# Performance work log

Measured on AMD Instinct MI355X. Metric: run time of the kernel, lower is better.

## Reference

```python
import math
import jax, jax.numpy as jnp
import numpy as np

E = 1024
H = 16
DH = E // H
R = 8
ALPHA = 16
LORA_S = ALPHA / R

def build_slopes(h):
    start = 2 ** (-2 ** (-(math.log2(h) - 3)))
    return jnp.asarray([start * start ** i for i in range(h)], dtype=jnp.float32)

def setup_inputs() -> dict:
    key = jax.random.key(0)
    ks = jax.random.split(key, 12)
    B, T = 2, 2048
    x = jax.random.normal(ks[0], (B, T, E), dtype=jnp.float32)
    # nn.Linear weights: [out_f, in_f]; LoRA A: [out_f, r], B: [r, in_f]
    def lin(k):
        return jax.random.normal(k, (E, E), dtype=jnp.float32) / math.sqrt(E)
    inp = {
        "x": x,
        "Wq": lin(ks[1]), "Aq": jax.random.normal(ks[2], (E, R)) * 0.01, "Bq": jax.random.normal(ks[3], (R, E)) * 0.01,
        "Wk": lin(ks[4]), "Ak": jax.random.normal(ks[5], (E, R)) * 0.01, "Bk": jax.random.normal(ks[6], (R, E)) * 0.01,
        "Wv": lin(ks[7]), "Av": jax.random.normal(ks[8], (E, R)) * 0.01, "Bv": jax.random.normal(ks[9], (R, E)) * 0.01,
        "Wp": lin(ks[10]),
    }
    return inp

def _lora(x, W, A, Bm):
    # x @ W.T + (x @ B.T) @ A.T * s
    return x @ W.T + ((x @ Bm.T) @ A.T) * LORA_S

def reference(x, Wq, Aq, Bq, Wk, Ak, Bk, Wv, Av, Bv, Wp):
    B, T, _ = x.shape
    slopes = build_slopes(H)  # [H]
    q = _lora(x, Wq, Aq, Bq).reshape(B, T, H, DH).transpose(0, 2, 1, 3)  # [B,H,T,dh]
    k = _lora(x, Wk, Ak, Bk).reshape(B, T, H, DH).transpose(0, 2, 1, 3)
    v = _lora(x, Wv, Av, Bv).reshape(B, T, H, DH).transpose(0, 2, 1, 3)
    s = jnp.einsum("bhqd,bhkd->bhqk", q, k) / math.sqrt(DH)
    i = jnp.arange(T, dtype=jnp.float32)[:, None]
    j = jnp.arange(T, dtype=jnp.float32)[None, :]
    alibi = slopes[:, None, None] * (i - j)  # [H,T,T]
    mask = jnp.triu(jnp.full((T, T), -jnp.inf, dtype=jnp.float32), 1)
    s = s + alibi[None] + mask
    p = jax.nn.softmax(s, axis=-1)
    o = jnp.einsum("bhqk,bhkd->bhqd", p, v).transpose(0, 2, 1, 3).reshape(B, T, E)
    return o @ Wp.T
```

## Files before the change

### kernel.cpp

```cpp
#include <hip/hip_runtime.h>

typedef unsigned short u16;
typedef unsigned int   u32;
typedef __bf16 bf16_t;
typedef bf16_t bf16x8 __attribute__((ext_vector_type(8)));
typedef bf16_t bf16x2v __attribute__((ext_vector_type(2)));
typedef float  f32x4  __attribute__((ext_vector_type(4)));

#define E_DIM 1024
#define T_DIM 2048
#define H_NUM 16
#define DH 64
#define BT 4096
#define Y_LD 2048

__device__ __forceinline__ u16 f2bf(float f) {
  u32 u = __builtin_bit_cast(u32, f);
  u32 r = (u + 0x7fffu + ((u >> 16) & 1u)) >> 16;
  return (u16)r;
}
__device__ __forceinline__ float bf2f(u16 v) {
  u32 u = ((u32)v) << 16;
  return __builtin_bit_cast(float, u);
}

__device__ __forceinline__ float fexp2(float x) {
#if __has_builtin(__builtin_amdgcn_exp2f)
  return __builtin_amdgcn_exp2f(x);
#else
  return exp2f(x);
#endif
}

__device__ __forceinline__ int swz(int r, int c) {
  return r * 64 + (c ^ ((r & 7) << 3));
}

typedef __attribute__((address_space(3))) unsigned int as3_u32;
typedef const __attribute__((address_space(1))) unsigned int as1_u32;

__device__ __forceinline__ void async16(const u16* g, u16* l) {
  __builtin_amdgcn_global_load_lds((as1_u32*)g, (as3_u32*)l, 16, 0, 0);
}

__device__ __forceinline__ void waitvm0_barrier() {
  asm volatile("s_waitcnt vmcnt(0)" ::: "memory");
  __builtin_amdgcn_s_barrier();
  __builtin_amdgcn_sched_barrier(0);
}

__device__ __forceinline__ void waitall_barrier() {
  asm volatile("s_waitcnt vmcnt(0) lgkmcnt(0)" ::: "memory");
  __builtin_amdgcn_s_barrier();
  __builtin_amdgcn_sched_barrier(0);
}

__device__ __forceinline__ u32 pack2(float a, float b) {
  bf16x2v v;
  v[0] = (bf16_t)a;
  v[1] = (bf16_t)b;
  return __builtin_bit_cast(u32, v);
}

__device__ __forceinline__ void plswap(u32& a, u32& b) {
#if __has_builtin(__builtin_amdgcn_permlane32_swap)
  typedef u32 u32x2 __attribute__((ext_vector_type(2)));
  u32x2 r = __builtin_amdgcn_permlane32_swap(a, b, false, false);
  a = r[0];
  b = r[1];
#else
  asm volatile("v_permlane32_swap_b32 %0, %1" : "+v"(a), "+v"(b));
#endif
}

__device__ __forceinline__ void redist_pair(u32 A, u32 B, bool odd, u32& wj, u32& wj2) {
  plswap(A, B);
  u32 sA = __builtin_amdgcn_ds_swizzle(A, 0x401F);
  u32 sB = __builtin_amdgcn_ds_swizzle(B, 0x401F);
  wj  = odd ? sB : A;
  wj2 = odd ? B : sA;
}

__global__ __launch_bounds__(256) void k_prep(
    const float* __restrict__ x,
    const float* __restrict__ W0, const float* __restrict__ A0, const float* __restrict__ B0,
    const float* __restrict__ W1, const float* __restrict__ A1, const float* __restrict__ B1,
    const float* __restrict__ W2, const float* __restrict__ A2, const float* __restrict__ B2,
    const float* __restrict__ Wp,
    u16* __restrict__ xb, u16* __restrict__ Weff, u16* __restrict__ Wpb, float s0) {
  const int blk = blockIdx.x;
  const int tid = threadIdx.x;
  if (blk < 4096) {
    int i = (blk * 256 + tid) * 4;
    float4 v = *reinterpret_cast<const float4*>(x + i);
    u32 lo = (u32)f2bf(v.x) | ((u32)f2bf(v.y) << 16);
    u32 hi = (u32)f2bf(v.z) | ((u32)f2bf(v.w) << 16);
    *reinterpret_cast<uint2*>(xb + i) = make_uint2(lo, hi);
  } else if (blk < 7168) {
    int e4 = (blk - 4096) * 256 + tid;
    int m = e4 >> 18;
    int e = (e4 & 262143) * 4;
    const float* W  = (m == 0) ? W0 : (m == 1) ? W1 : W2;
    const float* A  = (m == 0) ? A0 : (m == 1) ? A1 : A2;
    const float* Bm = (m == 0) ? B0 : (m == 1) ? B1 : B2;
    const float sc  = (m == 0) ? s0 : 1.0f;
    int o = e >> 10, i = e & 1023;
    float4 wv = *reinterpret_cast<const float4*>(W + e);
    float acc[4] = {wv.x, wv.y, wv.z, wv.w};
#pragma unroll
    for (int r = 0; r < 8; ++r) {
      float a2 = 2.0f * A[o * 8 + r];
      float4 bv = *reinterpret_cast<const float4*>(Bm + r * 1024 + i);
      acc[0] += a2 * bv.x; acc[1] += a2 * bv.y; acc[2] += a2 * bv.z; acc[3] += a2 * bv.w;
    }
    u32 lo = (u32)f2bf(acc[0] * sc) | ((u32)f2bf(acc[1] * sc) << 16);
    u32 hi = (u32)f2bf(acc[2] * sc) | ((u32)f2bf(acc[3] * sc) << 16);
    *reinterpret_cast<uint2*>(Weff + (size_t)m * 1048576 + e) = make_uint2(lo, hi);
  } else {
    int i = ((blk - 7168) * 256 + tid) * 4;
    float4 v = *reinterpret_cast<const float4*>(Wp + i);
    u32 lo = (u32)f2bf(v.x) | ((u32)f2bf(v.y) << 16);
    u32 hi = (u32)f2bf(v.z) | ((u32)f2bf(v.w) << 16);
    *reinterpret_cast<uint2*>(Wpb + i) = make_uint2(lo, hi);
  }
}

__global__ __launch_bounds__(512) void k_gemm2(
    const u16* __restrict__ A, const u16* __restrict__ B,
    u16* __restrict__ C, u16* __restrict__ Vt, int K, int ldc) {
  __shared__ __align__(16) u16 As[2][8192];
  __shared__ __align__(16) u16 Bs[2][8192];
  const int tid  = threadIdx.x;
  const int lane = tid & 63;
  const int wave = tid >> 6;
  const int wr = wave >> 2;
  const int wc = wave & 3;
  const int m0 = blockIdx.y * 128;
  const int n0 = blockIdx.x * 128;
  const int lr = lane & 15;
  const int lk = (lane >> 4) * 8;
  const bool vmode = (n0 >= 2048);

  f32x4 acc[4][2] = {};

  auto stageg = [&](int bufi, int t) {
#pragma unroll
    for (int p = 0; p < 2; ++p) {
      const int off = (p * 8 + wave) * 512;
      const int e = off + lane * 8;
      const int r = e >> 6, c = e & 63;
      const int cs = c ^ ((r & 7) << 3);
      async16(&A[(size_t)(m0 + r) * K + t * 64 + cs], &As[bufi][off]);
      async16(&B[(size_t)(n0 + r) * K + t * 64 + cs], &Bs[bufi][off]);
    }
  };

  const int nt = K >> 6;
  stageg(0, 0);
  waitvm0_barrier();
  int buf = 0;

  for (int t = 0; t < nt; ++t) {
    if (t + 1 < nt) stageg(buf ^ 1, t + 1);
    __builtin_amdgcn_s_setprio(1);
#pragma unroll
    for (int kk = 0; kk < 2; ++kk) {
      bf16x8 af[4], bfr[2];
#pragma unroll
      for (int mi = 0; mi < 4; ++mi)
        af[mi] = *reinterpret_cast<const bf16x8*>(&As[buf][swz(wr * 64 + mi * 16 + lr, kk * 32 + lk)]);
#pragma unroll
      for (int ni = 0; ni < 2; ++ni)
        bfr[ni] = *reinterpret_cast<const bf16x8*>(&Bs[buf][swz(wc * 32 + ni * 16 + lr, kk * 32 + lk)]);
      if (vmode) {
#pragma unroll
        for (int mi = 0; mi < 4; ++mi)
#pragma unroll
          for (int ni = 0; ni < 2; ++ni)
            acc[mi][ni] = __builtin_amdgcn_mfma_f32_16x16x32_bf16(bfr[ni], af[mi], acc[mi][ni], 0, 0, 0);
      } else {
#pragma unroll
        for (int mi = 0; mi < 4; ++mi)
#pragma unroll
          for (int ni = 0; ni < 2; ++ni)
            acc[mi][ni] = __builtin_amdgcn_mfma_f32_16x16x32_bf16(af[mi], bfr[ni], acc[mi][ni], 0, 0, 0);
      }
    }
    __builtin_amdgcn_s_setprio(0);
    waitvm0_barrier();
    buf ^= 1;
  }

  const int rg = (lane >> 4) * 4;
  if (vmode) {
#pragma unroll
    for (int mi = 0; mi < 4; ++mi)
#pragma unroll
      for (int ni = 0; ni < 2; ++ni)
#pragma unroll
        for (int q = 0; q < 4; ++q) {
          int o = n0 - 2048 + wc * 32 + ni * 16 + rg + q;
          int h = o >> 6, d = o & 63;
          int rowm = m0 + wr * 64 + mi * 16 + lr;
          int b = rowm >> 11, t = rowm & 2047;
          Vt[(size_t)(((b << 4) + h) * 64 + d) * 2048 + t] = f2bf(acc[mi][ni][q]);
        }
  } else {
#pragma unroll
    for (int mi = 0; mi < 4; ++mi)
#pragma unroll
      for (int ni = 0; ni < 2; ++ni)
#pragma unroll
        for (int q = 0; q < 4; ++q) {
          int row = m0 + wr * 64 + mi * 16 + rg + q;
          int col = n0 + wc * 32 + ni * 16 + lr;
          C[(size_t)row * ldc + col] = f2bf(acc[mi][ni][q]);
        }
  }
}

__global__ __launch_bounds__(512) void k_projm(
    const u16* __restrict__ Og, const u16* __restrict__ Oa, const u16* __restrict__ Ob,
    const float* __restrict__ la, const float* __restrict__ lb,
    const u16* __restrict__ B, float* __restrict__ C) {
  __shared__ __align__(16) u16 As[2][8192];
  __shared__ __align__(16) u16 Bs[2][8192];
  const int tid  = threadIdx.x;
  const int lane = tid & 63;
  const int wave = tid >> 6;
  const int wr = wave >> 2, wc = wave & 3;
  const int m0 = blockIdx.y * 128;
  const int n0 = blockIdx.x * 128;
  const int lr = lane & 15;
  const int lk = (lane >> 4) * 8;
  const bool upper = (m0 & 2047) >= 1024;
  const int K = 1024;

  f32x4 acc[4][2] = {};

  auto stageg = [&](int bufi, int t) {
#pragma unroll
    for (int p = 0; p < 2; ++p) {
      const int off = (p * 8 + wave) * 512;
      const int e = off + lane * 8;
      const int r = e >> 6, c = e & 63;
      const int cs = c ^ ((r & 7) << 3);
      async16(&B[(size_t)(n0 + r) * K + t * 64 + cs], &Bs[bufi][off]);
      if (!upper) {
        async16(&Og[(size_t)(m0 + r) * K + t * 64 + cs], &As[bufi][off]);
      } else {
        const int rowg = m0 + r;
        const int bb = rowg >> 11, tl = (rowg & 2047) - 1024;
        const int li = (bb * 16 + t) * 1024 + tl;
        const float inv = 1.0f / (la[li] + lb[li]);
        size_t po = (size_t)(bb * 1024 + tl) * 1024 + t * 64 + cs;
        uint4 va = *reinterpret_cast<const uint4*>(Oa + po);
        uint4 vb = *reinterpret_cast<const uint4*>(Ob + po);
        const u16* pa = reinterpret_cast<const u16*>(&va);
        const u16* pb = reinterpret_cast<const u16*>(&vb);
        u16 o[8];
#pragma unroll
        for (int j = 0; j < 8; ++j) o[j] = f2bf((bf2f(pa[j]) + bf2f(pb[j])) * inv);
        *reinterpret_cast<uint4*>(&As[bufi][off + lane * 8]) =
            *reinterpret_cast<const uint4*>(o);
      }
    }
  };

  const int nt = K >> 6;
  stageg(0, 0);
  waitall_barrier();
  int buf = 0;

  for (int t = 0; t < nt; ++t) {
    if (t + 1 < nt) stageg(buf ^ 1, t + 1);
    __builtin_amdgcn_s_setprio(1);
#pragma unroll
    for (int kk = 0; kk < 2; ++kk) {
      bf16x8 af[4], bfr[2];
#pragma unroll
      for (int mi = 0; mi < 4; ++mi)
        af[mi] = *reinterpret_cast<const bf16x8*>(&As[buf][swz(wr * 64 + mi * 16 + lr, kk * 32 + lk)]);
#pragma unroll
      for (int ni = 0; ni < 2; ++ni)
        bfr[ni] = *reinterpret_cast<const bf16x8*>(&Bs[buf][swz(wc * 32 + ni * 16 + lr, kk * 32 + lk)]);
#pragma unroll
      for (int mi = 0; mi < 4; ++mi)
#pragma unroll
        for (int ni = 0; ni < 2; ++ni)
          acc[mi][ni] = __builtin_amdgcn_mfma_f32_16x16x32_bf16(af[mi], bfr[ni], acc[mi][ni], 0, 0, 0);
    }
    __builtin_amdgcn_s_setprio(0);
    waitall_barrier();
    buf ^= 1;
  }

  const int rg = (lane >> 4) * 4;
#pragma unroll
  for (int mi = 0; mi < 4; ++mi)
#pragma unroll
    for (int ni = 0; ni < 2; ++ni)
#pragma unroll
      for (int q = 0; q < 4; ++q) {
        int row = m0 + wr * 64 + mi * 16 + rg + q;
        int col = n0 + wc * 32 + ni * 16 + lr;
        C[(size_t)row * 1024 + col] = acc[mi][ni][q];
      }
}

__global__ __launch_bounds__(256) void k_attn8(
    const u16* __restrict__ Y, const u16* __restrict__ Vt, u16* __restrict__ Og,
    u16* __restrict__ Oa, u16* __restrict__ Ob,
    float* __restrict__ la, float* __restrict__ lb) {
  __shared__ __align__(16) u16 Ks[2][4096];
  __shared__ __align__(16) u16 Vs[2][4096];

  const int tid = threadIdx.x;
  const int lane = tid & 63;
  const int wave = tid >> 6;
  const int lr = lane & 15;
  const int lg = lane >> 4;
  const int lk = lg * 8;
  const bool odd = (lane & 16) != 0;

  const int orig = blockIdx.x;
  const int h   = 15 - (orig / 96);
  const int rem = orig % 96;
  const int c   = rem >> 1;
  const int b   = rem & 1;
  const int bh  = b * 16 + h;
  const int qt = (c < 16) ? (16 + c) : (47 - c);
  const int ks = (c >= 16 && c < 32) ? 16 : 0;
  int ke       = (c < 16) ? 15 : qt;

  const float LOG2E = 1.4426950408889634f;
  const float slope2 = exp2f(-0.5f * (float)(h + 1)) * LOG2E;

  const int Th = min(32, (int)(64.0f / slope2) / 64 + 1);
  ke = min(ke, Th - 1);

  if (ks > ke) {
    const int base = b * 1024 + (qt * 64 - 1024);
#pragma unroll
    for (int p = 0; p < 2; ++p) {
      int idx = p * 256 + tid;
      int rr = idx >> 3, cc8 = (idx & 7) * 8;
      uint4 z = {0, 0, 0, 0};
      *reinterpret_cast<uint4*>(&Ob[(size_t)(base + rr) * E_DIM + h * DH + cc8]) = z;
    }
    if (tid < 64) lb[bh * 1024 + (qt * 64 - 1024) + tid] = 0.f;
    return;
  }

  const u16* Kb = Y + (size_t)b * T_DIM * Y_LD + 1024 + h * DH;
  const u16* Vb = Vt + (size_t)bh * DH * T_DIM;

  bf16x8 qf[2];
  {
    const int qrow = qt * 64 + wave * 16 + lr;
#pragma unroll
    for (int kk = 0; kk < 2; ++kk)
      qf[kk] = *reinterpret_cast<const bf16x8*>(
          &Y[(size_t)(b * T_DIM + qrow) * Y_LD + h * DH + kk * 32 + lk]);
  }

  float nkb[16];
#pragma unroll
  for (int ni = 0; ni < 4; ++ni)
#pragma unroll
    for (int r = 0; r < 4; ++r)
      nkb[ni * 4 + r] = -slope2 * (float)(ni * 16 + lg * 4 + r) - 12.0f;

  bf16x8 ones;
#pragma unroll
  for (int jj = 0; jj < 8; ++jj) ones[jj] = (bf16_t)1.0f;

  f32x4 oacc[4] = {};
  f32x4 lacc = {};

  auto stage = [&](int bufi, int kt) {
    const int kv0 = kt * 64;
#pragma unroll
    for (int q = 0; q < 2; ++q) {
      const int off = (q * 4 + wave) * 512;
      const int e = off + lane * 8;
      const int r = e >> 6, cc = e & 63;
      const int cs = cc ^ ((r & 7) << 3);
      async16(Kb + (size_t)(kv0 + r) * Y_LD + cs, &Ks[bufi][off]);
      async16(Vb + (size_t)r * T_DIM + kv0 + cs, &Vs[bufi][off]);
    }
  };

  auto step = [&](int kt, int buf, bool DIAG) {
    f32x4 s[4] = {};
    __builtin_amdgcn_s_setprio(1);
#pragma unroll
    for (int kk = 0; kk < 2; ++kk)
#pragma unroll
      for (int ni = 0; ni < 4; ++ni) {
        bf16x8 kf = *reinterpret_cast<const bf16x8*>(&Ks[buf][swz(ni * 16 + lr, kk * 32 + lk)]);
        s[ni] = __builtin_amdgcn_mfma_f32_16x16x32_bf16(kf, qf[kk], s[ni], 0, 0, 0);
      }
    __builtin_amdgcn_s_setprio(0);
    const float ck = -slope2 * (float)(kt * 64);
    u32 pk[4][2];
#pragma unroll
    for (int ni = 0; ni < 4; ++ni) {
      float p[4];
#pragma unroll
      for (int r = 0; r < 4; ++r) {
        float sc = s[ni][r] + nkb[ni * 4 + r] + ck;
        if (DIAG && (ni * 16 + lg * 4 + r) > (wave * 16 + lr)) sc = -INFINITY;
        p[r] = fexp2(sc);
      }
      pk[ni][0] = pack2(p[0], p[1]);
      pk[ni][1] = pack2(p[2], p[3]);
    }
    uint4 PW[2];
#pragma unroll
    for (int kk = 0; kk < 2; ++kk) {
      redist_pair(pk[2 * kk][0], pk[2 * kk + 1][0], odd, PW[kk].x, PW[kk].z);
      redist_pair(pk[2 * kk][1], pk[2 * kk + 1][1], odd, PW[kk].y, PW[kk].w);
    }
    __builtin_amdgcn_s_setprio(1);
#pragma unroll
    for (int kk = 0; kk < 2; ++kk) {
      bf16x8 ph = __builtin_bit_cast(bf16x8, PW[kk]);
      lacc = __builtin_amdgcn_mfma_f32_16x16x32_bf16(ph, ones, lacc, 0, 0, 0);
#pragma unroll
      for (int f = 0; f < 4; ++f) {
        bf16x8 vf = *reinterpret_cast<const bf16x8*>(&Vs[buf][swz(f * 16 + lr, kk * 32 + lk)]);
        oacc[f] = __builtin_amdgcn_mfma_f32_16x16x32_bf16(ph, vf, oacc[f], 0, 0, 0);
      }
    }
    __builtin_amdgcn_s_setprio(0);
  };

  stage(0, ks);
  waitvm0_barrier();
  int buf = 0;
  for (int kt = ks; kt <= ke; ++kt) {
    if (kt < ke) stage(buf ^ 1, kt + 1);
    step(kt, buf, kt == qt);
    waitvm0_barrier();
    buf ^= 1;
  }

  if (c >= 32) {
    float linv[4];
#pragma unroll
    for (int r = 0; r < 4; ++r) linv[r] = 1.0f / lacc[r];
#pragma unroll
    for (int f = 0; f < 4; ++f)
#pragma unroll
      for (int r = 0; r < 4; ++r) {
        int q = qt * 64 + wave * 16 + lg * 4 + r;
        Og[(size_t)(b * T_DIM + q) * E_DIM + h * DH + f * 16 + lr] =
            f2bf(oacc[f][r] * linv[r]);
      }
  } else {
    u16* Op   = (c < 16) ? Oa : Ob;
    float* lp = (c < 16) ? la : lb;
#pragma unroll
    for (int f = 0; f < 4; ++f)
#pragma unroll
      for (int r = 0; r < 4; ++r) {
        int q = qt * 64 + wave * 16 + lg * 4 + r;
        Op[(size_t)(b * 1024 + (q - 1024)) * E_DIM + h * DH + f * 16 + lr] =
            f2bf(oacc[f][r]);
      }
    if (lr == 0) {
#pragma unroll
      for (int r = 0; r < 4; ++r) {
        int q = qt * 64 + wave * 16 + lg * 4 + r;
        lp[bh * 1024 + (q - 1024)] = lacc[r];
      }
    }
  }
}

extern "C" void kernel_launch(void* const* d_in, const int* in_sizes, int n_in,
                              void* d_out, int out_size, void* d_ws, size_t ws_size,
                              hipStream_t stream) {
  const float* x  = (const float*)d_in[0];
  const float* Wq = (const float*)d_in[1];
  const float* Aq = (const float*)d_in[2];
  const float* Bq = (const float*)d_in[3];
  const float* Wk = (const float*)d_in[4];
  const float* Ak = (const float*)d_in[5];
  const float* Bk = (const float*)d_in[6];
  const float* Wv = (const float*)d_in[7];
  const float* Av = (const float*)d_in[8];
  const float* Bv = (const float*)d_in[9];
  const float* Wp = (const float*)d_in[10];
  float* out = (float*)d_out;

  char* ws = (char*)d_ws;
  const size_t MB = 1048576;
  u16* xb   = (u16*)(ws);
  u16* Oa   = (u16*)(ws);
  u16* Ob   = (u16*)(ws + 4 * MB);
  u16* Weff = (u16*)(ws + 8 * MB);
  float* la = (float*)(ws + 8 * MB);
  float* lb = (float*)(ws + 8 * MB + 131072);
  u16* Yq   = (u16*)(ws + 14 * MB);
  u16* VtB  = (u16*)(ws + 30 * MB);
  u16* Wpb  = (u16*)(ws + 38 * MB);
  u16* Og   = (u16*)(ws + 40 * MB);

  const float ISQ2 = 0.125f * 1.4426950408889634f;

  k_prep<<<8192, 256, 0, stream>>>(x, Wq, Aq, Bq, Wk, Ak, Bk, Wv, Av, Bv, Wp,
                                   xb, Weff, Wpb, ISQ2);
  {
    dim3 grid(24, 32);
    k_gemm2<<<grid, 512, 0, stream>>>(xb, Weff, Yq, VtB, E_DIM, Y_LD);
  }
  k_attn8<<<1536, 256, 0, stream>>>(Yq, VtB, Og, Oa, Ob, la, lb);
  {
    dim3 grid(8, 32);
    k_projm<<<grid, 512, 0, stream>>>(Og, Oa, Ob, la, lb, Wpb, out);
  }
}
```

Before: 107.7 us.

## Triple-buffer attention K/V staging and halve output-projection tile width

The attention kernel moves from double to triple-buffered K/V tiles in shared memory, prefetching two tiles ahead and waiting with vmcnt(4) so that one tile's loads can stay in flight across the barrier. The output projection kernel switches from 128-wide to 64-wide N tiles, doubling the grid to 512 blocks for better CU occupancy on a grid that was small. In exchange, attention uses more LDS per block, which may reduce occupancy. The narrower projection tiles recompute the A-side Oa/Ob merge twice as often and load A twice as often.

```diff
diff --git a/kernel.cpp b/kernel.cpp
--- a/kernel.cpp
+++ b/kernel.cpp
@@ -45,6 +45,12 @@
 
 __device__ __forceinline__ void waitvm0_barrier() {
   asm volatile("s_waitcnt vmcnt(0)" ::: "memory");
+  __builtin_amdgcn_s_barrier();
+  __builtin_amdgcn_sched_barrier(0);
+}
+
+__device__ __forceinline__ void waitvm4_barrier() {
+  asm volatile("s_waitcnt vmcnt(4)" ::: "memory");
   __builtin_amdgcn_s_barrier();
   __builtin_amdgcn_sched_barrier(0);
 }
@@ -224,28 +230,34 @@
     const float* __restrict__ la, const float* __restrict__ lb,
     const u16* __restrict__ B, float* __restrict__ C) {
   __shared__ __align__(16) u16 As[2][8192];
-  __shared__ __align__(16) u16 Bs[2][8192];
+  __shared__ __align__(16) u16 Bs[2][4096];
   const int tid  = threadIdx.x;
   const int lane = tid & 63;
   const int wave = tid >> 6;
   const int wr = wave >> 2, wc = wave & 3;
   const int m0 = blockIdx.y * 128;
-  const int n0 = blockIdx.x * 128;
+  const int n0 = blockIdx.x * 64;
   const int lr = lane & 15;
   const int lk = (lane >> 4) * 8;
   const bool upper = (m0 & 2047) >= 1024;
   const int K = 1024;
 
-  f32x4 acc[4][2] = {};
+  f32x4 acc[4][1] = {};
 
   auto stageg = [&](int bufi, int t) {
+    {
+      const int off = wave * 512;
+      const int e = off + lane * 8;
+      const int r = e >> 6, c = e & 63;
+      const int cs = c ^ ((r & 7) << 3);
+      async16(&B[(size_t)(n0 + r) * K + t * 64 + cs], &Bs[bufi][off]);
+    }
 #pragma unroll
     for (int p = 0; p < 2; ++p) {
       const int off = (p * 8 + wave) * 512;
       const int e = off + lane * 8;
       const int r = e >> 6, c = e & 63;
       const int cs = c ^ ((r & 7) << 3);
-      async16(&B[(size_t)(n0 + r) * K + t * 64 + cs], &Bs[bufi][off]);
       if (!upper) {
         async16(&Og[(size_t)(m0 + r) * K + t * 64 + cs], &As[bufi][off]);
       } else {
@@ -277,18 +289,14 @@
     __builtin_amdgcn_s_setprio(1);
 #pragma unroll
     for (int kk = 0; kk < 2; ++kk) {
-      bf16x8 af[4], bfr[2];
+      bf16x8 af[4], bfr;
 #pragma unroll
       for (int mi = 0; mi < 4; ++mi)
         af[mi] = *reinterpret_cast<const bf16x8*>(&As[buf][swz(wr * 64 + mi * 16 + lr, kk * 32 + lk)]);
-#pragma unroll
-      for (int ni = 0; ni < 2; ++ni)
-        bfr[ni] = *reinterpret_cast<const bf16x8*>(&Bs[buf][swz(wc * 32 + ni * 16 + lr, kk * 32 + lk)]);
+      bfr = *reinterpret_cast<const bf16x8*>(&Bs[buf][swz(wc * 16 + lr, kk * 32 + lk)]);
 #pragma unroll
       for (int mi = 0; mi < 4; ++mi)
-#pragma unroll
-        for (int ni = 0; ni < 2; ++ni)
-          acc[mi][ni] = __builtin_amdgcn_mfma_f32_16x16x32_bf16(af[mi], bfr[ni], acc[mi][ni], 0, 0, 0);
+        acc[mi][0] = __builtin_amdgcn_mfma_f32_16x16x32_bf16(af[mi], bfr, acc[mi][0], 0, 0, 0);
     }
     __builtin_amdgcn_s_setprio(0);
     waitall_barrier();
@@ -299,21 +307,19 @@
 #pragma unroll
   for (int mi = 0; mi < 4; ++mi)
 #pragma unroll
-    for (int ni = 0; ni < 2; ++ni)
-#pragma unroll
-      for (int q = 0; q < 4; ++q) {
-        int row = m0 + wr * 64 + mi * 16 + rg + q;
-        int col = n0 + wc * 32 + ni * 16 + lr;
-        C[(size_t)row * 1024 + col] = acc[mi][ni][q];
-      }
+    for (int q = 0; q < 4; ++q) {
+      int row = m0 + wr * 64 + mi * 16 + rg + q;
+      int col = n0 + wc * 16 + lr;
+      C[(size_t)row * 1024 + col] = acc[mi][0][q];
+    }
 }
 
 __global__ __launch_bounds__(256) void k_attn8(
     const u16* __restrict__ Y, const u16* __restrict__ Vt, u16* __restrict__ Og,
     u16* __restrict__ Oa, u16* __restrict__ Ob,
     float* __restrict__ la, float* __restrict__ lb) {
-  __shared__ __align__(16) u16 Ks[2][4096];
-  __shared__ __align__(16) u16 Vs[2][4096];
+  __shared__ __align__(16) u16 Ks[3][4096];
+  __shared__ __align__(16) u16 Vs[3][4096];
 
   const int tid = threadIdx.x;
   const int lane = tid & 63;
@@ -437,13 +443,22 @@
   };
 
   stage(0, ks);
-  waitvm0_barrier();
-  int buf = 0;
+  if (ks + 1 <= ke) {
+    stage(1, ks + 1);
+    waitvm4_barrier();
+  } else {
+    waitvm0_barrier();
+  }
+
   for (int kt = ks; kt <= ke; ++kt) {
-    if (kt < ke) stage(buf ^ 1, kt + 1);
+    const int buf = (kt - ks) % 3;
+    const bool pf = (kt + 2 <= ke);
+    if (pf) stage((kt - ks + 2) % 3, kt + 2);
     step(kt, buf, kt == qt);
-    waitvm0_barrier();
-    buf ^= 1;
+    if (kt < ke) {
+      if (pf) waitvm4_barrier();
+      else    waitvm0_barrier();
+    }
   }
 
   if (c >= 32) {
@@ -518,7 +533,7 @@
   }
   k_attn8<<<1536, 256, 0, stream>>>(Yq, VtB, Og, Oa, Ob, la, lb);
   {
-    dim3 grid(8, 32);
+    dim3 grid(16, 32);
     k_projm<<<grid, 512, 0, stream>>>(Og, Oa, Ob, la, lb, Wpb, out);
   }
 }
```

Result: slower. 113.5 us (+5.3%).
